# Kernel optimization log

Hardware: AMD Instinct MI355X
Metric: run time of the kernel (lower is better)

## Reference

```python
import jax, jax.numpy as jnp
import numpy as np

B, L, H, E = 32, 256, 8, 16
SEQ_LEN = 64          # init seq_len, used only in final view
OUT = 256             # out_channels, must be divisible by SEQ_LEN
A = E + 1 + 128       # augmented channels: original + time + conv(128)
SIG_CH = A + A * A    # depth-2 signature channels
DN = ('NWC', 'WIO', 'NWC')


def setup_inputs() -> dict:
    key = jax.random.key(0)
    ks = jax.random.split(key, 8)
    return {
        'q': jax.random.normal(ks[0], (B, L, H, E), jnp.float32),
        'k': jax.random.normal(ks[1], (B, L, H, E), jnp.float32),
        'v': jax.random.normal(ks[2], (B, L, H, E), jnp.float32),
        'mask': jnp.zeros((B, L), jnp.bool_),
        'conv1_w': jax.random.normal(ks[3], (3, E, 64), jnp.float32) * 0.1,
        'conv1_b': jnp.zeros((64,), jnp.float32),
        'conv2_w': jax.random.normal(ks[4], (1, 64, 128), jnp.float32) * 0.1,
        'conv2_b': jnp.zeros((128,), jnp.float32),
        'lin_w': jax.random.normal(ks[5], (SIG_CH, OUT), jnp.float32) * 0.01,
        'lin_b': jnp.zeros((OUT,), jnp.float32),
    }


def _signature_depth2(p):
    # p: [N, S, C] piecewise-linear path. Returns [N, C + C*C].
    dx = p[:, 1:] - p[:, :-1]                       # [N, S-1, C]
    s1 = dx.sum(axis=1)                             # level 1
    cum_excl = jnp.cumsum(dx, axis=1) - dx          # sum of increments before t
    # level 2: sum_{s<t} dx_s (x) dx_t + 0.5 * dx_t (x) dx_t
    s2 = jnp.einsum('nti,ntj->nij', cum_excl + 0.5 * dx, dx)
    return jnp.concatenate([s1, s2.reshape(s2.shape[0], -1)], axis=-1)


def reference(q, k, v, mask, conv1_w, conv1_b, conv2_w, conv2_b, lin_w, lin_b):
    Bq, Lq, Hq, Eq = q.shape
    x = q.transpose(0, 2, 1, 3).reshape(Bq * Hq, Lq, Eq)   # [N, L, E]
    T = Lq - 3 + 1                                          # valid-conv length, kernel 3
    # Augment pieces
    trunc = x[:, 2:]                                        # [N, T, E]
    time = jnp.broadcast_to(jnp.linspace(0.0, 1.0, T, dtype=x.dtype)[None, :, None],
                            (Bq * Hq, T, 1))
    a = jax.lax.conv_general_dilated(x, conv1_w, (1,), 'VALID', dimension_numbers=DN) + conv1_b
    a = jax.nn.relu(jax.lax.conv_general_dilated(a, conv2_w, (1,), 'VALID', dimension_numbers=DN) + conv2_b)
    aug = jnp.concatenate([trunc, time, a], axis=2)         # [N, T, A]
    # lead-lag transform as written in source: interleave along time -> [N, 2T, A]
    lag = jnp.concatenate([aug[:, 1:], aug[:, -1:]], axis=1)
    ll = jnp.stack([aug, lag], axis=2).reshape(aug.shape[0], 2 * T, aug.shape[2])
    sig = _signature_depth2(ll)                             # [N, SIG_CH]
    out = sig @ lin_w + lin_b                               # [N, OUT]
    return out.reshape(Bq, Hq, SEQ_LEN, -1)
```

## Files before the change

kernel.cpp:

```cpp
#include <hip/hip_runtime.h>
#include <hip/hip_bf16.h>

#define Bq 32
#define Lq 256
#define Hq 8
#define Eq 16
#define Nn (Bq*Hq)
#define T 254
#define A 145
#define SIG_CH (A + A*A)
#define KP 21184
#define OUT 256

typedef __attribute__((ext_vector_type(8))) short short8;
typedef __attribute__((ext_vector_type(8))) unsigned short ushort8;
typedef __attribute__((ext_vector_type(4))) float floatx4;

static __device__ __forceinline__ unsigned short f2bf(float v) {
    unsigned int u = __float_as_uint(v);
    unsigned int r = (u + 0x7FFFu + ((u >> 16) & 1u)) >> 16;
    return (unsigned short)r;
}
static __device__ __forceinline__ float bf2f(unsigned short b) {
    return __uint_as_float(((unsigned int)b) << 16);
}

#define MDS 40
#define OS3 36
#define XIS 72
#define GRPB 61600
#define ACS 162

__global__ __launch_bounds__(512) void augsig_kernel(
    const float* __restrict__ q,
    const float* __restrict__ b1, const float* __restrict__ b2,
    const float* __restrict__ w1, const float* __restrict__ w2,
    unsigned short* __restrict__ sig_hi, unsigned short* __restrict__ sig_lo)
{
    __shared__ __align__(16) char smem[2*GRPB + 256 + 512 + 640 + 640];

    const int tid512 = threadIdx.x;
    const int grp = tid512 >> 8;
    const int tid = tid512 & 255;

    char* gb = smem + grp*GRPB;
    unsigned short* mdb = (unsigned short*)gb;
    float* outs = (float*)(gb + 38400);
    float* xsc  = (float*)(gb + 59280);
    float* b1s  = (float*)(smem + 2*GRPB);
    float* b2s  = b1s + 64;
    float* a0s  = b2s + 128;
    float* vls  = a0s + 160;
    float* accs = (float*)smem;

    unsigned short* Mh = mdb;
    unsigned short* Ml = mdb + 160*MDS;
    unsigned short* Dh = mdb + 2*160*MDS;
    unsigned short* ximh = mdb;
    unsigned short* ximl = mdb + 3456;
    unsigned short* a1h  = mdb + 6912;
    unsigned short* a1l  = mdb + 10368;

    const int n = blockIdx.x;
    const int b = n >> 3, h = n & 7;

    const int lane = tid & 63;
    const int wv   = tid >> 6;
    const int frow = lane & 15;
    const int quad = lane >> 4;
    const int wm = wv & 1, wn = wv >> 1;

    if (tid512 < 64)  b1s[tid512] = b1[tid512];
    if (tid512 < 128) b2s[tid512] = b2[tid512];

    const float4* q4 = (const float4*)q + ((long)(b*Lq)*Hq + h)*4;
    const float inv253 = 1.0f / 253.0f;

    float4 rq0, rq1, rq2, rq3;
    if (tid < 140) {
        const int r = tid >> 2, e4 = tid & 3;
        int t;
        t = (0*2 + grp)*32 + r; if (t > 255) t = 255; rq0 = q4[t*32 + e4];
        t = (1*2 + grp)*32 + r; if (t > 255) t = 255; rq1 = q4[t*32 + e4];
        t = (2*2 + grp)*32 + r; if (t > 255) t = 255; rq2 = q4[t*32 + e4];
        t = (3*2 + grp)*32 + r; if (t > 255) t = 255; rq3 = q4[t*32 + e4];
    }

    short8 c1bh[2], c1bl[2];
    {
        const int cch = wv*16 + frow;
        #pragma unroll
        for (int ks = 0; ks < 2; ++ks) {
            unsigned short hb8[8], lb8[8];
            #pragma unroll
            for (int e = 0; e < 8; ++e) {
                int k = ks*32 + quad*8 + e;
                float v = (k < 48) ? w1[k*64 + cch] : 0.f;
                unsigned short hbv = f2bf(v);
                hb8[e] = hbv; lb8[e] = f2bf(v - bf2f(hbv));
            }
            c1bh[ks] = *(short8*)hb8; c1bl[ks] = *(short8*)lb8;
        }
    }
    short8 c2bh[2][2], c2bl[2][2];
    #pragma unroll
    for (int nt = 0; nt < 2; ++nt) {
        const int cch = wv*32 + nt*16 + frow;
        #pragma unroll
        for (int ks = 0; ks < 2; ++ks) {
            unsigned short hb8[8], lb8[8];
            #pragma unroll
            for (int e = 0; e < 8; ++e) {
                int i = ks*32 + quad*8 + e;
                float v = w2[i*128 + cch];
                unsigned short hbv = f2bf(v);
                hb8[e] = hbv; lb8[e] = f2bf(v - bf2f(hbv));
            }
            c2bh[nt][ks] = *(short8*)hb8; c2bl[nt][ks] = *(short8*)lb8;
        }
    }

    floatx4 acc[5][5];
    #pragma unroll
    for (int i = 0; i < 5; ++i)
        #pragma unroll
        for (int j = 0; j < 5; ++j)
            acc[i][j] = (floatx4){0.f, 0.f, 0.f, 0.f};

    #pragma unroll 1
    for (int ci = 0; ci < 4; ++ci) {
        const int c = 2*ci + grp;
        const int t0 = c*32;

        if (tid < 140) {
            float4 qv = (ci == 0) ? rq0 : (ci == 1) ? rq1 : (ci == 2) ? rq2 : rq3;
            ((float4*)xsc)[tid] = qv;
        }
        __syncthreads();

        for (int idx = tid; idx < 48*8; idx += 256) {
            int r = idx >> 3, g = idx & 7;
            unsigned short hh[8], ll[8];
            if (r <= 32 && g < 6) {
                const float* src = &xsc[r*16 + g*8];
                #pragma unroll
                for (int e = 0; e < 8; ++e) {
                    float v = src[e];
                    unsigned short hbv = f2bf(v);
                    hh[e] = hbv; ll[e] = f2bf(v - bf2f(hbv));
                }
            } else {
                #pragma unroll
                for (int e = 0; e < 8; ++e) { hh[e] = 0; ll[e] = 0; }
            }
            *(ushort8*)&ximh[r*XIS + g*8] = *(ushort8*)hh;
            *(ushort8*)&ximl[r*XIS + g*8] = *(ushort8*)ll;
        }
        __syncthreads();

        {
            short8 ah[3][2], al[3][2];
            #pragma unroll
            for (int mt = 0; mt < 3; ++mt)
                #pragma unroll
                for (int ks = 0; ks < 2; ++ks) {
                    int ar = (mt*16 + frow)*XIS + ks*32 + quad*8;
                    ah[mt][ks] = *(const short8*)&ximh[ar];
                    al[mt][ks] = *(const short8*)&ximl[ar];
                }
            floatx4 acc1[3];
            #pragma unroll
            for (int mt = 0; mt < 3; ++mt) acc1[mt] = (floatx4){0.f,0.f,0.f,0.f};
            #pragma unroll
            for (int mt = 0; mt < 3; ++mt)
                #pragma unroll
                for (int ks = 0; ks < 2; ++ks) {
                    acc1[mt] = __builtin_amdgcn_mfma_f32_16x16x32_bf16(ah[mt][ks], c1bh[ks], acc1[mt], 0,0,0);
                    acc1[mt] = __builtin_amdgcn_mfma_f32_16x16x32_bf16(ah[mt][ks], c1bl[ks], acc1[mt], 0,0,0);
                    acc1[mt] = __builtin_amdgcn_mfma_f32_16x16x32_bf16(al[mt][ks], c1bh[ks], acc1[mt], 0,0,0);
                }
            const int cc = wv*16 + frow;
            const float bias = b1s[cc];
            #pragma unroll
            for (int mt = 0; mt < 3; ++mt)
                #pragma unroll
                for (int e = 0; e < 4; ++e) {
                    int t = mt*16 + quad*4 + e;
                    float v = acc1[mt][e] + bias;
                    unsigned short hbv = f2bf(v);
                    a1h[t*XIS + cc] = hbv;
                    a1l[t*XIS + cc] = f2bf(v - bf2f(hbv));
                }
        }
        __syncthreads();

        {
            short8 ah[3][2], al[3][2];
            #pragma unroll
            for (int mt = 0; mt < 3; ++mt)
                #pragma unroll
                for (int ks = 0; ks < 2; ++ks) {
                    int ar = (mt*16 + frow)*XIS + ks*32 + quad*8;
                    ah[mt][ks] = *(const short8*)&a1h[ar];
                    al[mt][ks] = *(const short8*)&a1l[ar];
                }
            floatx4 acc2[3][2];
            #pragma unroll
            for (int mt = 0; mt < 3; ++mt)
                #pragma unroll
                for (int nt = 0; nt < 2; ++nt)
                    acc2[mt][nt] = (floatx4){0.f,0.f,0.f,0.f};
            #pragma unroll
            for (int mt = 0; mt < 3; ++mt)
                #pragma unroll
                for (int nt = 0; nt < 2; ++nt)
                    #pragma unroll
                    for (int ks = 0; ks < 2; ++ks) {
                        acc2[mt][nt] = __builtin_amdgcn_mfma_f32_16x16x32_bf16(ah[mt][ks], c2bh[nt][ks], acc2[mt][nt], 0,0,0);
                        acc2[mt][nt] = __builtin_amdgcn_mfma_f32_16x16x32_bf16(ah[mt][ks], c2bl[nt][ks], acc2[mt][nt], 0,0,0);
                        acc2[mt][nt] = __builtin_amdgcn_mfma_f32_16x16x32_bf16(al[mt][ks], c2bh[nt][ks], acc2[mt][nt], 0,0,0);
                    }
            #pragma unroll
            for (int mt = 0; mt < 3; ++mt)
                #pragma unroll
                for (int nt = 0; nt < 2; ++nt) {
                    int cc = wv*32 + nt*16 + frow;
                    float bias = b2s[cc];
                    int tb = mt*16 + quad*4;
                    if (tb <= 32) {
                        float4 vv;
                        vv.x = fmaxf(acc2[mt][nt][0] + bias, 0.f);
                        vv.y = fmaxf(acc2[mt][nt][1] + bias, 0.f);
                        vv.z = fmaxf(acc2[mt][nt][2] + bias, 0.f);
                        vv.w = fmaxf(acc2[mt][nt][3] + bias, 0.f);
                        *(float4*)&outs[(17 + cc)*OS3 + tb] = vv;
                    }
                }
        }
        for (int idx = tid; idx < 17*33; idx += 256) {
            int ch = idx / 33, tt = idx - ch*33;
            float val = (ch < 16) ? xsc[(tt+2)*16 + ch] : (float)(t0+tt)*inv253;
            outs[ch*OS3 + tt] = val;
        }
        __syncthreads();

        for (int task = tid; task < 290; task += 256) {
            int ch = task >> 1, hh2 = task & 1;
            const float* orow = &outs[ch*OS3 + hh2*16];
            float v[17];
            float4 va = *(const float4*)&orow[0];
            float4 vb = *(const float4*)&orow[4];
            float4 vc = *(const float4*)&orow[8];
            float4 vd = *(const float4*)&orow[12];
            v[0]=va.x; v[1]=va.y; v[2]=va.z; v[3]=va.w;
            v[4]=vb.x; v[5]=vb.y; v[6]=vb.z; v[7]=vb.w;
            v[8]=vc.x; v[9]=vc.y; v[10]=vc.z; v[11]=vc.w;
            v[12]=vd.x; v[13]=vd.y; v[14]=vd.z; v[15]=vd.w;
            v[16] = orow[16];
            if (c == 0 && hh2 == 0) a0s[ch] = v[0];
            if (c == 7 && hh2 == 1) vls[ch] = v[13];
            unsigned short mh[16], ml[16], dh[16];
            const int tbase = t0 + hh2*16;
            #pragma unroll
            for (int tl = 0; tl < 16; ++tl) {
                bool valid = (tbase + tl) <= 252;
                float x0 = v[tl], x1 = v[tl+1];
                float d = valid ? (x1 - x0) : 0.f;
                float m = valid ? (0.5f*(x0 + x1)) : 0.f;
                unsigned short hbv = f2bf(m);
                mh[tl] = hbv; ml[tl] = f2bf(m - bf2f(hbv));
                dh[tl] = f2bf(d);
            }
            int mo = ch*MDS + hh2*16;
            *(ushort8*)&Mh[mo]     = *(ushort8*)&mh[0];
            *(ushort8*)&Mh[mo + 8] = *(ushort8*)&mh[8];
            *(ushort8*)&Ml[mo]     = *(ushort8*)&ml[0];
            *(ushort8*)&Ml[mo + 8] = *(ushort8*)&ml[8];
            *(ushort8*)&Dh[mo]     = *(ushort8*)&dh[0];
            *(ushort8*)&Dh[mo + 8] = *(ushort8*)&dh[8];
        }
        __syncthreads();

        {
            short8 afh[5], afl[5], bfh[5];
            #pragma unroll
            for (int i = 0; i < 5; ++i) {
                int ar = (wm*80 + i*16 + frow)*MDS + quad*8;
                int br = (wn*80 + i*16 + frow)*MDS + quad*8;
                afh[i] = *(const short8*)&Mh[ar];
                afl[i] = *(const short8*)&Ml[ar];
                bfh[i] = *(const short8*)&Dh[br];
            }
            #pragma unroll
            for (int mt = 0; mt < 5; ++mt)
                #pragma unroll
                for (int nt = 0; nt < 5; ++nt) {
                    acc[mt][nt] = __builtin_amdgcn_mfma_f32_16x16x32_bf16(
                        afh[mt], bfh[nt], acc[mt][nt], 0, 0, 0);
                    acc[mt][nt] = __builtin_amdgcn_mfma_f32_16x16x32_bf16(
                        afl[mt], bfh[nt], acc[mt][nt], 0, 0, 0);
                }
        }
    }

    __syncthreads();

    if (grp == 1) {
        #pragma unroll
        for (int mt = 0; mt < 5; ++mt)
            #pragma unroll
            for (int nt = 0; nt < 5; ++nt) {
                int j = wn*80 + nt*16 + frow;
                int ib = wm*80 + mt*16 + quad*4;
                #pragma unroll
                for (int e = 0; e < 4; ++e)
                    accs[(ib + e)*ACS + j] = acc[mt][nt][e];
            }
    }
    __syncthreads();

    if (grp == 0) {
        #pragma unroll
        for (int mt = 0; mt < 5; ++mt)
            #pragma unroll
            for (int nt = 0; nt < 5; ++nt) {
                int j = wn*80 + nt*16 + frow;
                int ib = wm*80 + mt*16 + quad*4;
                float s1j = (j < A) ? (vls[j] - a0s[j]) : 0.f;
                #pragma unroll
                for (int e = 0; e < 4; ++e) {
                    int i = ib + e;
                    float a0i = (i < A) ? a0s[i] : 0.f;
                    accs[i*ACS + j] = acc[mt][nt][e] + accs[i*ACS + j] - a0i*s1j;
                }
            }
    }
    __syncthreads();

    unsigned short* sh = sig_hi + (long)n*KP;
    unsigned short* sl = sig_lo + (long)n*KP;

    if (tid512 < 290) {
        const int r = tid512 >> 1, hh2 = tid512 & 1;
        const float* row = accs + r*ACS;
        const long g0 = (long)A + (long)r*A;
        const int s0 = (8 - (int)(g0 & 7)) & 7;
        if (hh2 == 0) {
            for (int j = 0; j < s0; ++j) {
                float v = row[j];
                unsigned short hbv = f2bf(v);
                sh[g0 + j] = hbv;
                sl[g0 + j] = f2bf(v - bf2f(hbv));
            }
            for (int vb8 = 0; vb8 < 8; ++vb8) {
                int j0 = s0 + vb8*8;
                unsigned short hb8[8], lb8[8];
                #pragma unroll
                for (int e = 0; e < 8; ++e) {
                    float v = row[j0 + e];
                    unsigned short hbv = f2bf(v);
                    hb8[e] = hbv; lb8[e] = f2bf(v - bf2f(hbv));
                }
                *(ushort8*)(sh + g0 + j0) = *(ushort8*)hb8;
                *(ushort8*)(sl + g0 + j0) = *(ushort8*)lb8;
            }
        } else {
            int j0 = s0 + 64;
            for (; j0 + 8 <= A; j0 += 8) {
                unsigned short hb8[8], lb8[8];
                #pragma unroll
                for (int e = 0; e < 8; ++e) {
                    float v = row[j0 + e];
                    unsigned short hbv = f2bf(v);
                    hb8[e] = hbv; lb8[e] = f2bf(v - bf2f(hbv));
                }
                *(ushort8*)(sh + g0 + j0) = *(ushort8*)hb8;
                *(ushort8*)(sl + g0 + j0) = *(ushort8*)lb8;
            }
            for (; j0 < A; ++j0) {
                float v = row[j0];
                unsigned short hbv = f2bf(v);
                sh[g0 + j0] = hbv;
                sl[g0 + j0] = f2bf(v - bf2f(hbv));
            }
        }
    } else if (tid512 < 290 + A) {
        int ch = tid512 - 290;
        float v = vls[ch] - a0s[ch];
        unsigned short hbv = f2bf(v);
        sh[ch] = hbv;
        sl[ch] = f2bf(v - bf2f(hbv));
    } else if (tid512 < 290 + A + (KP - SIG_CH)) {
        int p = tid512 - (290 + A);
        sh[SIG_CH + p] = 0;
        sl[SIG_CH + p] = 0;
    }
}

#define SPLITK 111
#define KC 192
#define NSTEP (KC/32)
#define LDA 40

__global__ __launch_bounds__(256) void gemm_kernel(
    const unsigned short* __restrict__ sig_hi, const unsigned short* __restrict__ sig_lo,
    const float* __restrict__ W,
    float* __restrict__ part)
{
    __shared__ __align__(16) unsigned short Ah[128*LDA];
    __shared__ __align__(16) unsigned short Al[128*LDA];
    __shared__ __align__(16) unsigned short Bh[64*LDA];
    __shared__ __align__(16) unsigned short Bl[64*LDA];

    const int tid = threadIdx.x;
    const int lin  = blockIdx.x + 4*blockIdx.y + 8*blockIdx.z;
    const int lin2 = (lin & 7)*SPLITK + (lin >> 3);
    const int z  = lin2 >> 3;
    const int m  = lin2 & 7;
    const int o0 = (m & 3) * 64;
    const int n0 = (m >> 2) * 128;
    const int k0 = z * KC;

    const int lane = tid & 63;
    const int w    = tid >> 6;
    const int wm   = w & 1;
    const int wn   = w >> 1;
    const int frow = lane & 15;
    const int quad = lane >> 4;

    const int srowA = tid >> 1;
    const int khA   = (tid & 1) * 16;
    const int oo    = tid & 63;
    const int ks8   = tid >> 6;

    const unsigned short* gAh = sig_hi + (long)(n0 + srowA)*KP;
    const unsigned short* gAl = sig_lo + (long)(n0 + srowA)*KP;
    const float*          gB  = W + (o0 + oo);

    ushort8 rah[2], ral[2];
    float wv8[8];
    const ushort8 z8 = {0,0,0,0,0,0,0,0};

    #define GLOAD(s)                                                          \
        {                                                                     \
            int kb = k0 + (s)*32;                                             \
            if (kb < KP) {                                                    \
                rah[0] = *(const ushort8*)(gAh + kb + khA);                   \
                rah[1] = *(const ushort8*)(gAh + kb + khA + 8);               \
                ral[0] = *(const ushort8*)(gAl + kb + khA);                   \
                ral[1] = *(const ushort8*)(gAl + kb + khA + 8);               \
            } else {                                                          \
                rah[0]=z8; rah[1]=z8; ral[0]=z8; ral[1]=z8;                   \
            }                                                                 \
            int kbb = kb + ks8*8;                                             \
            _Pragma("unroll")                                                 \
            for (int j = 0; j < 8; ++j) {                                     \
                int k = kbb + j;                                              \
                wv8[j] = (k < SIG_CH) ? gB[(long)k*OUT] : 0.f;                \
            }                                                                 \
        }

    #define LSTORE()                                                          \
        {                                                                     \
            int oA = srowA*LDA + khA;                                         \
            *(ushort8*)(Ah + oA)     = rah[0];                                \
            *(ushort8*)(Ah + oA + 8) = rah[1];                                \
            *(ushort8*)(Al + oA)     = ral[0];                                \
            *(ushort8*)(Al + oA + 8) = ral[1];                                \
            unsigned short hb8[8], lb8[8];                                    \
            _Pragma("unroll")                                                 \
            for (int j = 0; j < 8; ++j) {                                     \
                unsigned short hbv = f2bf(wv8[j]);                            \
                hb8[j] = hbv; lb8[j] = f2bf(wv8[j] - bf2f(hbv));              \
            }                                                                 \
            int oB = oo*LDA + ks8*8;                                          \
            *(ushort8*)(Bh + oB) = *(ushort8*)hb8;                            \
            *(ushort8*)(Bl + oB) = *(ushort8*)lb8;                            \
        }

    floatx4 acc[4][2];
    #pragma unroll
    for (int i = 0; i < 4; ++i)
        #pragma unroll
        for (int j = 0; j < 2; ++j)
            acc[i][j] = (floatx4){0.f, 0.f, 0.f, 0.f};

    GLOAD(0);
    LSTORE();
    __syncthreads();

    for (int s = 0; s < NSTEP; ++s) {
        if (s < NSTEP-1) GLOAD(s+1);

        short8 afh[4], afl[4], bfh[2], bfl[2];
        const int aoff = (wm*64 + frow)*LDA + quad*8;
        const int boff = (wn*32 + frow)*LDA + quad*8;
        #pragma unroll
        for (int tI = 0; tI < 4; ++tI) {
            afh[tI] = *(const short8*)(Ah + aoff + tI*16*LDA);
            afl[tI] = *(const short8*)(Al + aoff + tI*16*LDA);
        }
        #pragma unroll
        for (int tI = 0; tI < 2; ++tI) {
            bfh[tI] = *(const short8*)(Bh + boff + tI*16*LDA);
            bfl[tI] = *(const short8*)(Bl + boff + tI*16*LDA);
        }
        #pragma unroll
        for (int mt = 0; mt < 4; ++mt)
            #pragma unroll
            for (int nt = 0; nt < 2; ++nt) {
                acc[mt][nt] = __builtin_amdgcn_mfma_f32_16x16x32_bf16(
                    afh[mt], bfh[nt], acc[mt][nt], 0, 0, 0);
                acc[mt][nt] = __builtin_amdgcn_mfma_f32_16x16x32_bf16(
                    afh[mt], bfl[nt], acc[mt][nt], 0, 0, 0);
                acc[mt][nt] = __builtin_amdgcn_mfma_f32_16x16x32_bf16(
                    afl[mt], bfh[nt], acc[mt][nt], 0, 0, 0);
            }
        __syncthreads();
        if (s < NSTEP-1) {
            LSTORE();
            __syncthreads();
        }
    }

    float* pz = part + (long)z * (Nn*OUT);
    #pragma unroll
    for (int mt = 0; mt < 4; ++mt)
        #pragma unroll
        for (int nt = 0; nt < 2; ++nt) {
            int col = o0 + wn*32 + nt*16 + frow;
            int rbase = n0 + wm*64 + mt*16 + quad*4;
            #pragma unroll
            for (int e = 0; e < 4; ++e)
                pz[(long)(rbase + e)*OUT + col] = acc[mt][nt][e];
        }
}

__global__ __launch_bounds__(256) void reduce_kernel(
    const float* __restrict__ part, const float* __restrict__ lb,
    float* __restrict__ out)
{
    int idx = blockIdx.x * 256 + threadIdx.x;
    float s = lb[idx & 255];
    #pragma unroll 8
    for (int z = 0; z < SPLITK; ++z)
        s += part[(long)z * (Nn*OUT) + idx];
    out[idx] = s;
}

extern "C" void kernel_launch(void* const* d_in, const int* in_sizes, int n_in,
                              void* d_out, int out_size, void* d_ws, size_t ws_size,
                              hipStream_t stream) {
    const float* q  = (const float*)d_in[0];
    const float* w1 = (const float*)d_in[4];
    const float* b1 = (const float*)d_in[5];
    const float* w2 = (const float*)d_in[6];
    const float* b2 = (const float*)d_in[7];
    const float* lw = (const float*)d_in[8];
    const float* lb = (const float*)d_in[9];
    float* out = (float*)d_out;

    char* ws = (char*)d_ws;
    unsigned short* sig_hi  = (unsigned short*)ws;
    unsigned short* sig_lo  = (unsigned short*)(ws + 10846208);
    float*          part    = (float*)(ws + 21692416);

    augsig_kernel<<<Nn, 512, 0, stream>>>(q, b1, b2, w1, w2, sig_hi, sig_lo);
    gemm_kernel<<<dim3(4, 2, SPLITK), 256, 0, stream>>>(sig_hi, sig_lo, lw, part);
    reduce_kernel<<<(Nn*OUT)/256, 256, 0, stream>>>(part, lb, out);
}
```

Measured before the change: 154.6 us.

## Load GEMM fragments directly from global into registers, dropping LDS staging

The split-K GEMM stops staging A and B tiles through shared memory. Each wave now loads its MFMA fragments straight from global memory into a double-buffered register set, and converts W to bf16 hi/lo in registers, so the loop needs no __syncthreads. The K chunk per block grows from 192 to 256, which cuts split-K partials from 111 to 83, and launch bounds request 2 blocks per SM. The cost is redundant global loads, since two waves share each A row and W is read uncoalesced with a stride of OUT. Register pressure also rises.

New measurement: 166.3 us. +7.6%, slower.

```diff
diff --git a/kernel.cpp b/kernel.cpp
--- a/kernel.cpp
+++ b/kernel.cpp
@@ -397,21 +397,15 @@
     }
 }
 
-#define SPLITK 111
-#define KC 192
+#define SPLITK 83
+#define KC 256
 #define NSTEP (KC/32)
-#define LDA 40
-
-__global__ __launch_bounds__(256) void gemm_kernel(
+
+__global__ __launch_bounds__(256, 2) void gemm_kernel(
     const unsigned short* __restrict__ sig_hi, const unsigned short* __restrict__ sig_lo,
     const float* __restrict__ W,
     float* __restrict__ part)
 {
-    __shared__ __align__(16) unsigned short Ah[128*LDA];
-    __shared__ __align__(16) unsigned short Al[128*LDA];
-    __shared__ __align__(16) unsigned short Bh[64*LDA];
-    __shared__ __align__(16) unsigned short Bl[64*LDA];
-
     const int tid = threadIdx.x;
     const int lin  = blockIdx.x + 4*blockIdx.y + 8*blockIdx.z;
     const int lin2 = (lin & 7)*SPLITK + (lin >> 3);
@@ -428,54 +422,70 @@
     const int frow = lane & 15;
     const int quad = lane >> 4;
 
-    const int srowA = tid >> 1;
-    const int khA   = (tid & 1) * 16;
-    const int oo    = tid & 63;
-    const int ks8   = tid >> 6;
-
-    const unsigned short* gAh = sig_hi + (long)(n0 + srowA)*KP;
-    const unsigned short* gAl = sig_lo + (long)(n0 + srowA)*KP;
-    const float*          gB  = W + (o0 + oo);
-
-    ushort8 rah[2], ral[2];
-    float wv8[8];
-    const ushort8 z8 = {0,0,0,0,0,0,0,0};
-
-    #define GLOAD(s)                                                          \
+    const long arow0 = (long)(n0 + wm*64 + frow)*KP + quad*8;
+    const int  ocol  = o0 + wn*32 + frow;
+    const int  kq    = quad*8;
+
+    short8 afh0[4], afl0[4], afh1[4], afl1[4];
+    float  wf0[2][8], wf1[2][8];
+    const short8 z8s = {0,0,0,0,0,0,0,0};
+
+    #define LOADSTEP(SET, s_)                                                 \
         {                                                                     \
-            int kb = k0 + (s)*32;                                             \
+            const int kb = k0 + (s_)*32;                                      \
             if (kb < KP) {                                                    \
-                rah[0] = *(const ushort8*)(gAh + kb + khA);                   \
-                rah[1] = *(const ushort8*)(gAh + kb + khA + 8);               \
-                ral[0] = *(const ushort8*)(gAl + kb + khA);                   \
-                ral[1] = *(const ushort8*)(gAl + kb + khA + 8);               \
+                _Pragma("unroll")                                             \
+                for (int tI = 0; tI < 4; ++tI) {                              \
+                    long ro = arow0 + (long)tI*16*KP + kb;                    \
+                    afh##SET[tI] = *(const short8*)(sig_hi + ro);             \
+                    afl##SET[tI] = *(const short8*)(sig_lo + ro);             \
+                }                                                             \
+                _Pragma("unroll")                                             \
+                for (int tJ = 0; tJ < 2; ++tJ) {                              \
+                    _Pragma("unroll")                                         \
+                    for (int e = 0; e < 8; ++e) {                             \
+                        int k = kb + kq + e;                                  \
+                        wf##SET[tJ][e] = (k < SIG_CH)                         \
+                            ? W[(long)k*OUT + ocol + tJ*16] : 0.f;            \
+                    }                                                         \
+                }                                                             \
             } else {                                                          \
-                rah[0]=z8; rah[1]=z8; ral[0]=z8; ral[1]=z8;                   \
+                _Pragma("unroll")                                             \
+                for (int tI = 0; tI < 4; ++tI) {                              \
+                    afh##SET[tI] = z8s; afl##SET[tI] = z8s;                   \
+                }                                                             \
+                _Pragma("unroll")                                             \
+                for (int tJ = 0; tJ < 2; ++tJ)                                \
+                    _Pragma("unroll")                                         \
+                    for (int e = 0; e < 8; ++e) wf##SET[tJ][e] = 0.f;         \
             }                                                                 \
-            int kbb = kb + ks8*8;                                             \
-            _Pragma("unroll")                                                 \
-            for (int j = 0; j < 8; ++j) {                                     \
-                int k = kbb + j;                                              \
-                wv8[j] = (k < SIG_CH) ? gB[(long)k*OUT] : 0.f;                \
-            }                                                                 \
-        }
-
-    #define LSTORE()                                                          \
-        {                                                                     \
-            int oA = srowA*LDA + khA;                                         \
-            *(ushort8*)(Ah + oA)     = rah[0];                                \
-            *(ushort8*)(Ah + oA + 8) = rah[1];                                \
-            *(ushort8*)(Al + oA)     = ral[0];                                \
-            *(ushort8*)(Al + oA + 8) = ral[1];                                \
-            unsigned short hb8[8], lb8[8];                                    \
-            _Pragma("unroll")                                                 \
-            for (int j = 0; j < 8; ++j) {                                     \
-                unsigned short hbv = f2bf(wv8[j]);                            \
-                hb8[j] = hbv; lb8[j] = f2bf(wv8[j] - bf2f(hbv));              \
-            }                                                                 \
-            int oB = oo*LDA + ks8*8;                                          \
-            *(ushort8*)(Bh + oB) = *(ushort8*)hb8;                            \
-            *(ushort8*)(Bl + oB) = *(ushort8*)lb8;                            \
+        }
+
+    #define DOMFMA(SET)                                                      \
+        {                                                                    \
+            short8 bfh[2], bfl[2];                                           \
+            _Pragma("unroll")                                                \
+            for (int tJ = 0; tJ < 2; ++tJ) {                                 \
+                unsigned short hb8[8], lb8[8];                               \
+                _Pragma("unroll")                                            \
+                for (int e = 0; e < 8; ++e) {                                \
+                    unsigned short hbv = f2bf(wf##SET[tJ][e]);               \
+                    hb8[e] = hbv;                                            \
+                    lb8[e] = f2bf(wf##SET[tJ][e] - bf2f(hbv));               \
+                }                                                            \
+                bfh[tJ] = *(short8*)hb8; bfl[tJ] = *(short8*)lb8;            \
+            }                                                                \
+            _Pragma("unroll")                                                \
+            for (int mt = 0; mt < 4; ++mt)                                   \
+                _Pragma("unroll")                                            \
+                for (int nt = 0; nt < 2; ++nt) {                             \
+                    acc[mt][nt] = __builtin_amdgcn_mfma_f32_16x16x32_bf16(   \
+                        afh##SET[mt], bfh[nt], acc[mt][nt], 0, 0, 0);        \
+                    acc[mt][nt] = __builtin_amdgcn_mfma_f32_16x16x32_bf16(   \
+                        afh##SET[mt], bfl[nt], acc[mt][nt], 0, 0, 0);        \
+                    acc[mt][nt] = __builtin_amdgcn_mfma_f32_16x16x32_bf16(   \
+                        afl##SET[mt], bfh[nt], acc[mt][nt], 0, 0, 0);        \
+                }                                                            \
         }
 
     floatx4 acc[4][2];
@@ -485,42 +495,13 @@
         for (int j = 0; j < 2; ++j)
             acc[i][j] = (floatx4){0.f, 0.f, 0.f, 0.f};
 
-    GLOAD(0);
-    LSTORE();
-    __syncthreads();
-
-    for (int s = 0; s < NSTEP; ++s) {
-        if (s < NSTEP-1) GLOAD(s+1);
-
-        short8 afh[4], afl[4], bfh[2], bfl[2];
-        const int aoff = (wm*64 + frow)*LDA + quad*8;
-        const int boff = (wn*32 + frow)*LDA + quad*8;
-        #pragma unroll
-        for (int tI = 0; tI < 4; ++tI) {
-            afh[tI] = *(const short8*)(Ah + aoff + tI*16*LDA);
-            afl[tI] = *(const short8*)(Al + aoff + tI*16*LDA);
-        }
-        #pragma unroll
-        for (int tI = 0; tI < 2; ++tI) {
-            bfh[tI] = *(const short8*)(Bh + boff + tI*16*LDA);
-            bfl[tI] = *(const short8*)(Bl + boff + tI*16*LDA);
-        }
-        #pragma unroll
-        for (int mt = 0; mt < 4; ++mt)
-            #pragma unroll
-            for (int nt = 0; nt < 2; ++nt) {
-                acc[mt][nt] = __builtin_amdgcn_mfma_f32_16x16x32_bf16(
-                    afh[mt], bfh[nt], acc[mt][nt], 0, 0, 0);
-                acc[mt][nt] = __builtin_amdgcn_mfma_f32_16x16x32_bf16(
-                    afh[mt], bfl[nt], acc[mt][nt], 0, 0, 0);
-                acc[mt][nt] = __builtin_amdgcn_mfma_f32_16x16x32_bf16(
-                    afl[mt], bfh[nt], acc[mt][nt], 0, 0, 0);
-            }
-        __syncthreads();
-        if (s < NSTEP-1) {
-            LSTORE();
-            __syncthreads();
-        }
+    LOADSTEP(0, 0);
+    #pragma unroll
+    for (int s = 0; s < NSTEP; s += 2) {
+        LOADSTEP(1, s+1);
+        DOMFMA(0);
+        if (s + 2 < NSTEP) LOADSTEP(0, s+2);
+        DOMFMA(1);
     }
 
     float* pz = part + (long)z * (Nn*OUT);
```
